# Kernel tuning notes

Hardware: AMD Instinct MI355X
Metric: run time of the kernel (lower is better)

The kernel has to match this reference:

```python
import jax, jax.numpy as jnp
import numpy as np

B, L, D, C = 8, 1024, 512, 4  # batch, maxlen, input_units(=output_unit), channel


def setup_inputs() -> dict:
    key = jax.random.key(0)
    ks = jax.random.split(key, 6)
    scale = 1.0 / np.sqrt(D)  # glorot-ish
    inputs = jax.random.normal(ks[0], (B, L, D), dtype=jnp.float32)
    pad_k = jnp.zeros((B, L, 1), dtype=jnp.float32)  # 0 = valid, -99999 = pad
    w_l = jax.random.normal(ks[1], (C, D, D), dtype=jnp.float32) * scale   # scalar_w per channel
    b_l = jnp.zeros((C,), dtype=jnp.float32)                                # scalar_b per channel
    w_v1 = jax.random.normal(ks[2], (C, D), dtype=jnp.float32) * scale     # vector_w1 [D,1] squeezed
    w_v2 = jax.random.normal(ks[3], (C, D, D), dtype=jnp.float32) * scale  # vector_w2
    b_v = jnp.zeros((C, D), dtype=jnp.float32)                              # vector_b [1,1,D] squeezed
    return {"inputs": inputs, "pad_k": pad_k, "w_l": w_l, "b_l": b_l,
            "w_v1": w_v1, "w_v2": w_v2, "b_v": b_v}


def reference(inputs, pad_k, w_l, b_l, w_v1, w_v2, b_v):
    # inputs: [B,L,D], pad_k: [B,L,1]. Dropout (mask_prob) is identity at inference.
    pad_k2 = (pad_k + 99999.0) / 99999.0              # [B,L,1], 1 at valid, 0 at pad
    pk = pad_k[:, None, :, 0]                          # [B,1,L]

    # --- scalar (pairwise bilinear) attention, all channels at once ---
    mat_l = jnp.einsum('bld,cde->bcle', inputs, w_l)   # [B,C,L,D]
    # M[b,c,i,j] = sum_d inputs[b,i,d] * mat_l[b,c,j,d] + b_l[c]
    M = jnp.einsum('bid,bcjd->bcij', inputs, mat_l) + b_l[None, :, None, None]
    A = jnp.tanh(M)                                    # [B,C,L,L]
    s = A.sum(axis=3)                                  # sum over j -> [B,C,L]
    a = jax.nn.softmax(pk + s, axis=-1)[..., None]     # softmax over L -> [B,C,L,1]

    # --- vector attention ---
    sb = jnp.tanh(jnp.einsum('bld,cde->bcle', inputs, w_v2) + b_v[None, :, None, :])  # [B,C,L,D]
    score_bar = jnp.einsum('bcld,cd->bcl', sb, w_v1) + pk                              # [B,C,L]
    a_bar = jax.nn.softmax(score_bar, axis=-1)                                         # [B,C,L]
    pooled = jnp.einsum('bcl,bld->bcd', a_bar, inputs)                                 # [B,C,D]

    # C_l = a_l * inputs + pooled(broadcast over L) * pad_k2
    C_l = a * inputs[:, None] + pooled[:, :, None, :] * pad_k2[:, None]                # [B,C,L,D]

    C_features = jnp.concatenate(
        [jnp.transpose(C_l, (0, 2, 3, 1)), inputs[..., None]], axis=-1)                # [B,L,D,C+1]
    return C_features, a, a_bar[..., None]
```

## Files before the change

### kernel.cpp

```cpp
#include <hip/hip_runtime.h>

#define BB 8
#define LL 1024
#define DD 512
#define CC 4

typedef unsigned short u16;
typedef unsigned int u32;
typedef __attribute__((ext_vector_type(8))) short bf16x8;
typedef __attribute__((ext_vector_type(4))) float f32x4;
typedef __attribute__((ext_vector_type(4))) unsigned short u16x4;
typedef __attribute__((ext_vector_type(4))) float float4v;

typedef __attribute__((address_space(1))) const u32 gu32;
typedef __attribute__((address_space(3))) u32 lu32;
typedef __attribute__((address_space(3))) u16 l16;

__device__ __forceinline__ void gload16(const void* g, void* l) {
  __builtin_amdgcn_global_load_lds((gu32*)g, (lu32*)l, 16, 0, 0);
}
__device__ __forceinline__ u32 lds_off(const u16* p) {
  return (u32)(uintptr_t)(l16*)p;
}

__device__ __forceinline__ u16 f2bf(float f) {
  unsigned u = __float_as_uint(f);
  u += 0x7FFF + ((u >> 16) & 1);
  return (u16)(u >> 16);
}
__device__ __forceinline__ float bf2f(u16 h) {
  return __uint_as_float(((unsigned)h) << 16);
}
__device__ __forceinline__ float fast_tanh(float x) {
  return 1.0f - 2.0f / (__expf(2.0f * x) + 1.0f);
}

__global__ __launch_bounds__(256) void k_split(const float4v* __restrict__ x,
                                               u16* __restrict__ hi, u16* __restrict__ lo) {
  int i = blockIdx.x * 256 + threadIdx.x;
  float4v v = x[i];
  u16x4 h, l;
#pragma unroll
  for (int k = 0; k < 4; ++k) {
    u16 hh = f2bf(v[k]);
    h[k] = hh;
    l[k] = f2bf(v[k] - bf2f(hh));
  }
  *(u16x4*)&hi[(size_t)i * 4] = h;
  *(u16x4*)&lo[(size_t)i * 4] = l;
}

__global__ __launch_bounds__(256) void k_tsplit(const float* __restrict__ w,
                                                u16* __restrict__ thi, u16* __restrict__ tlo) {
  __shared__ float t[32][33];
  int c = blockIdx.z;
  int tx = threadIdx.x;
  int ty = threadIdx.y;
  int e0 = blockIdx.x * 32, d0 = blockIdx.y * 32;
#pragma unroll
  for (int k = 0; k < 32; k += 8)
    t[ty + k][tx] = w[((size_t)c * DD + d0 + ty + k) * DD + e0 + tx];
  __syncthreads();
#pragma unroll
  for (int k = 0; k < 32; k += 8) {
    float v = t[tx][ty + k];
    size_t o = ((size_t)c * DD + e0 + ty + k) * DD + d0 + tx;
    u16 h = f2bf(v);
    thi[o] = h;
    if (tlo) tlo[o] = f2bf(v - bf2f(h));
  }
}

#define DSR(dst, addr, OFF) \
  asm volatile("ds_read_b128 %0, %1 offset:" #OFF : "=v"(dst) : "v"(addr))
#define LGKM(N) \
  do { __builtin_amdgcn_sched_barrier(0); \
       asm volatile("s_waitcnt lgkmcnt(" #N ")" ::: "memory"); \
       __builtin_amdgcn_sched_barrier(0); } while (0)

template<int NSEG, bool SPLIT>
__device__ __forceinline__ void gemm256(const u16* __restrict__ Ahi, const u16* __restrict__ Alo,
                                        const u16* __restrict__ Bhi, const u16* __restrict__ Blo,
                                        u16* lA, u16* lB, f32x4 (&acc)[8][4]) {
  const int tid = threadIdx.x;
  const int lane = tid & 63;
  const int wave = tid >> 6;
  const int wr = wave >> 2, wc = wave & 3;
  const int fr = lane & 15;
  const int fq = lane >> 4;
  const int xs = (tid & 7) ^ ((tid >> 3) & 7);
  const size_t soff = (size_t)(tid >> 3) * DD + (size_t)xs * 8;
  const int p0 = fq ^ (fr & 7);
  const int dk = ((p0 ^ 4) - p0) * 16;
  const u32 ra = lds_off(lA) + (u32)((wr * 128 + fr) * 128 + p0 * 16);
  const u32 rb = lds_off(lB) + (u32)((wc * 64 + fr) * 128 + p0 * 16);

  const int NT = NSEG * 8;

#define STAGE_TOP(T, beo) do {                                                \
    const int seg_ = SPLIT ? ((T) >> 3) : 0;                                  \
    const int kp_ = ((T) & 7) * 64;                                           \
    const u16* As_ = (SPLIT && seg_ == 1) ? Alo : Ahi;                        \
    const u16* Bs_ = (SPLIT && seg_ == 2) ? Blo : Bhi;                        \
    gload16(As_ + soff + kp_,                 lA + (beo) + tid * 8);          \
    gload16(Bs_ + soff + kp_,                 lB + (beo) + tid * 8);          \
    gload16(As_ + soff + (size_t)64 * DD + kp_, lA + (beo) + tid * 8 + 4096); \
    gload16(Bs_ + soff + (size_t)64 * DD + kp_, lB + (beo) + tid * 8 + 4096); \
  } while (0)

#define STAGE_MID(T, beo) do {                                                \
    const int seg_ = SPLIT ? ((T) >> 3) : 0;                                  \
    const int kp_ = ((T) & 7) * 64;                                           \
    const u16* As_ = (SPLIT && seg_ == 1) ? Alo : Ahi;                        \
    const u16* Bs_ = (SPLIT && seg_ == 2) ? Blo : Bhi;                        \
    gload16(As_ + soff + (size_t)128 * DD + kp_, lA + (beo) + tid * 8 + 8192);  \
    gload16(Bs_ + soff + (size_t)128 * DD + kp_, lB + (beo) + tid * 8 + 8192);  \
    gload16(As_ + soff + (size_t)192 * DD + kp_, lA + (beo) + tid * 8 + 12288); \
    gload16(Bs_ + soff + (size_t)192 * DD + kp_, lB + (beo) + tid * 8 + 12288); \
  } while (0)

#define MFMA2(m0, m1) do {                                                    \
    _Pragma("unroll")                                                         \
    for (int ni = 0; ni < 4; ++ni)                                            \
      acc[m0][ni] = __builtin_amdgcn_mfma_f32_16x16x32_bf16(                  \
          af[m0], bv[ni], acc[m0][ni], 0, 0, 0);                              \
    _Pragma("unroll")                                                         \
    for (int ni = 0; ni < 4; ++ni)                                            \
      acc[m1][ni] = __builtin_amdgcn_mfma_f32_16x16x32_bf16(                  \
          af[m1], bv[ni], acc[m1][ni], 0, 0, 0);                              \
  } while (0)

#define HALF(aA_, aB_) do {                                                   \
    bf16x8 af[8], bv[4];                                                      \
    DSR(bv[0], aB_, 0);    DSR(bv[1], aB_, 2048);                             \
    DSR(bv[2], aB_, 4096); DSR(bv[3], aB_, 6144);                             \
    DSR(af[0], aA_, 0);    DSR(af[1], aA_, 2048);                             \
    DSR(af[2], aA_, 4096); DSR(af[3], aA_, 6144);                             \
    LGKM(2);                                                                  \
    MFMA2(0, 1);                                                              \
    DSR(af[4], aA_, 8192); DSR(af[5], aA_, 10240);                            \
    LGKM(2);                                                                  \
    MFMA2(2, 3);                                                              \
    DSR(af[6], aA_, 12288); DSR(af[7], aA_, 14336);                           \
    LGKM(2);                                                                  \
    MFMA2(4, 5);                                                              \
    LGKM(0);                                                                  \
    MFMA2(6, 7);                                                              \
  } while (0)

#define HALF_MID(aA_, aB_, T, beo) do {                                       \
    bf16x8 af[8], bv[4];                                                      \
    DSR(bv[0], aB_, 0);    DSR(bv[1], aB_, 2048);                             \
    DSR(bv[2], aB_, 4096); DSR(bv[3], aB_, 6144);                             \
    DSR(af[0], aA_, 0);    DSR(af[1], aA_, 2048);                             \
    DSR(af[2], aA_, 4096); DSR(af[3], aA_, 6144);                             \
    LGKM(2);                                                                  \
    MFMA2(0, 1);                                                              \
    DSR(af[4], aA_, 8192); DSR(af[5], aA_, 10240);                            \
    LGKM(2);                                                                  \
    MFMA2(2, 3);                                                              \
    STAGE_MID(T, beo);                                                        \
    DSR(af[6], aA_, 12288); DSR(af[7], aA_, 14336);                           \
    LGKM(2);                                                                  \
    MFMA2(4, 5);                                                              \
    LGKM(0);                                                                  \
    MFMA2(6, 7);                                                              \
  } while (0)

  STAGE_TOP(0, 0);
  STAGE_MID(0, 0);
  int beN = 16384;
  u32 bo = 0;
#pragma unroll 1
  for (int t = 0; t < NT - 1; ++t) {
    __builtin_amdgcn_sched_barrier(0);
    asm volatile("s_waitcnt vmcnt(0)" ::: "memory");
    __builtin_amdgcn_sched_barrier(0);
    __builtin_amdgcn_s_barrier();
    __builtin_amdgcn_sched_barrier(0);
    STAGE_TOP(t + 1, beN);
    {
      u32 aA0 = ra + bo, aB0 = rb + bo;
      __builtin_amdgcn_s_setprio(1);
      HALF_MID(aA0, aB0, t + 1, beN);
      u32 aA1 = aA0 + dk, aB1 = aB0 + dk;
      HALF(aA1, aB1);
      __builtin_amdgcn_s_setprio(0);
    }
    beN ^= 16384;
    bo ^= 32768u;
  }
  __builtin_amdgcn_sched_barrier(0);
  asm volatile("s_waitcnt vmcnt(0)" ::: "memory");
  __builtin_amdgcn_sched_barrier(0);
  __builtin_amdgcn_s_barrier();
  __builtin_amdgcn_sched_barrier(0);
  {
    u32 aA0 = ra + bo, aB0 = rb + bo;
    __builtin_amdgcn_s_setprio(1);
    HALF(aA0, aB0);
    u32 aA1 = aA0 + dk, aB1 = aB0 + dk;
    HALF(aA1, aB1);
    __builtin_amdgcn_s_setprio(0);
  }
#undef STAGE_TOP
#undef STAGE_MID
#undef HALF
#undef HALF_MID
#undef MFMA2
}

__global__ __launch_bounds__(512, 2) void k_matl(const u16* __restrict__ Xhi, const u16* __restrict__ Xlo,
                                                 const u16* __restrict__ Whi, const u16* __restrict__ Wlo,
                                                 u16* __restrict__ mhi, u16* __restrict__ mlo) {
  __shared__ u16 lA[2 * 256 * 64];
  __shared__ u16 lB[2 * 256 * 64];
  int lin = blockIdx.x;
  int virt = (lin & 7) * 32 + (lin >> 3);
  int bc = virt >> 3, rem = virt & 7;
  int tm = rem >> 1, tn = rem & 1;
  int b = bc >> 2, c = bc & 3;
  const u16* Ahi = Xhi + (size_t)b * LL * DD + (size_t)tm * 256 * DD;
  const u16* Alo = Xlo + (size_t)b * LL * DD + (size_t)tm * 256 * DD;
  const u16* Bhi = Whi + (size_t)c * DD * DD + (size_t)tn * 256 * DD;
  const u16* Blo = Wlo + (size_t)c * DD * DD + (size_t)tn * 256 * DD;
  f32x4 acc[8][4];
#pragma unroll
  for (int mi = 0; mi < 8; ++mi)
#pragma unroll
    for (int ni = 0; ni < 4; ++ni) acc[mi][ni] = (f32x4){0.f, 0.f, 0.f, 0.f};
  gemm256<3, true>(Ahi, Alo, Bhi, Blo, lA, lB, acc);

  int lane = threadIdx.x & 63, wave = threadIdx.x >> 6;
  int wr = wave >> 2, wc = wave & 3;
  int rgrp = (lane >> 4) * 4, cidx = lane & 15;
#pragma unroll
  for (int mi = 0; mi < 8; ++mi)
#pragma unroll
    for (int ni = 0; ni < 4; ++ni) {
      int row = tm * 256 + wr * 128 + mi * 16 + rgrp;
      int col = tn * 256 + wc * 64 + ni * 16 + cidx;
#pragma unroll
      for (int j = 0; j < 4; ++j) {
        float v = acc[mi][ni][j];
        size_t o = ((size_t)bc * LL + row + j) * DD + col;
        u16 h = f2bf(v);
        mhi[o] = h;
        mlo[o] = f2bf(v - bf2f(h));
      }
    }
}

__global__ __launch_bounds__(512, 2) void k_s(const u16* __restrict__ Xhi, const u16* __restrict__ Xlo,
                                              const u16* __restrict__ mhi, const u16* __restrict__ mlo,
                                              const float* __restrict__ b_l, float* __restrict__ s_part) {
  __shared__ u16 lA[2 * 256 * 64];
  __shared__ u16 lB[2 * 256 * 64];
  int lin = blockIdx.x;
  int virt = (lin & 7) * 64 + (lin >> 3);
  int bc = virt >> 4, rem = virt & 15;
  int tm = rem >> 2, tn = rem & 3;
  int b = bc >> 2, c = bc & 3;
  const u16* Ahi = Xhi + (size_t)b * LL * DD + (size_t)tm * 256 * DD;
  const u16* Alo = Xlo + (size_t)b * LL * DD + (size_t)tm * 256 * DD;
  const u16* Bhi = mhi + (size_t)bc * LL * DD + (size_t)tn * 256 * DD;
  const u16* Blo = mlo + (size_t)bc * LL * DD + (size_t)tn * 256 * DD;
  f32x4 acc[8][4];
#pragma unroll
  for (int mi = 0; mi < 8; ++mi)
#pragma unroll
    for (int ni = 0; ni < 4; ++ni) acc[mi][ni] = (f32x4){0.f, 0.f, 0.f, 0.f};
  gemm256<3, true>(Ahi, Alo, Bhi, Blo, lA, lB, acc);

  int lane = threadIdx.x & 63, wave = threadIdx.x >> 6;
  int wr = wave >> 2, wc = wave & 3;
  float bl = b_l[c];
  float part[8][4];
#pragma unroll
  for (int mi = 0; mi < 8; ++mi)
#pragma unroll
    for (int j = 0; j < 4; ++j) part[mi][j] = 0.f;
#pragma unroll
  for (int mi = 0; mi < 8; ++mi)
#pragma unroll
    for (int ni = 0; ni < 4; ++ni)
#pragma unroll
      for (int j = 0; j < 4; ++j) part[mi][j] += fast_tanh(acc[mi][ni][j] + bl);
#pragma unroll
  for (int mi = 0; mi < 8; ++mi)
#pragma unroll
    for (int j = 0; j < 4; ++j) {
      float v = part[mi][j];
      v += __shfl_xor(v, 1, 64);
      v += __shfl_xor(v, 2, 64);
      v += __shfl_xor(v, 4, 64);
      v += __shfl_xor(v, 8, 64);
      part[mi][j] = v;
    }
  if ((lane & 15) == 0) {
    int slot = bc * 16 + tn * 4 + wc;
    int rg = (lane >> 4) * 4;
#pragma unroll
    for (int mi = 0; mi < 8; ++mi)
#pragma unroll
      for (int j = 0; j < 4; ++j) {
        int row = tm * 256 + wr * 128 + mi * 16 + rg + j;
        s_part[(size_t)slot * LL + row] = part[mi][j];
      }
  }
}

__global__ __launch_bounds__(512, 2) void k_sbar(const u16* __restrict__ Xhi, const u16* __restrict__ Wv2T,
                                                 const float* __restrict__ b_v, const float* __restrict__ w_v1,
                                                 float* __restrict__ sc_part) {
  __shared__ u16 lA[2 * 256 * 64];
  __shared__ u16 lB[2 * 256 * 64];
  int lin = blockIdx.x;
  int virt = (lin & 7) * 32 + (lin >> 3);
  int bc = virt >> 3, rem = virt & 7;
  int tm = rem >> 1, tn = rem & 1;
  int b = bc >> 2, c = bc & 3;
  const u16* Ahi = Xhi + (size_t)b * LL * DD + (size_t)tm * 256 * DD;
  const u16* Bhi = Wv2T + (size_t)c * DD * DD + (size_t)tn * 256 * DD;
  f32x4 acc[8][4];
#pragma unroll
  for (int mi = 0; mi < 8; ++mi)
#pragma unroll
    for (int ni = 0; ni < 4; ++ni) acc[mi][ni] = (f32x4){0.f, 0.f, 0.f, 0.f};
  gemm256<1, false>(Ahi, nullptr, Bhi, nullptr, lA, lB, acc);

  int lane = threadIdx.x & 63, wave = threadIdx.x >> 6;
  int wr = wave >> 2, wc = wave & 3;
  int cidx = lane & 15;
  float wv[4], bvv[4];
#pragma unroll
  for (int ni = 0; ni < 4; ++ni) {
    int col = tn * 256 + wc * 64 + ni * 16 + cidx;
    wv[ni] = w_v1[c * DD + col];
    bvv[ni] = b_v[c * DD + col];
  }
  float part[8][4];
#pragma unroll
  for (int mi = 0; mi < 8; ++mi)
#pragma unroll
    for (int j = 0; j < 4; ++j) part[mi][j] = 0.f;
#pragma unroll
  for (int mi = 0; mi < 8; ++mi)
#pragma unroll
    for (int ni = 0; ni < 4; ++ni)
#pragma unroll
      for (int j = 0; j < 4; ++j) part[mi][j] += fast_tanh(acc[mi][ni][j] + bvv[ni]) * wv[ni];
#pragma unroll
  for (int mi = 0; mi < 8; ++mi)
#pragma unroll
    for (int j = 0; j < 4; ++j) {
      float v = part[mi][j];
      v += __shfl_xor(v, 1, 64);
      v += __shfl_xor(v, 2, 64);
      v += __shfl_xor(v, 4, 64);
      v += __shfl_xor(v, 8, 64);
      part[mi][j] = v;
    }
  if ((lane & 15) == 0) {
    int slot = bc * 8 + tn * 4 + wc;
    int rg = (lane >> 4) * 4;
#pragma unroll
    for (int mi = 0; mi < 8; ++mi)
#pragma unroll
      for (int j = 0; j < 4; ++j) {
        int row = tm * 256 + wr * 128 + mi * 16 + rg + j;
        sc_part[(size_t)slot * LL + row] = part[mi][j];
      }
  }
}

__device__ __forceinline__ float blk_max(float v, float* red, int tid) {
#pragma unroll
  for (int m = 32; m >= 1; m >>= 1) v = fmaxf(v, __shfl_xor(v, m, 64));
  if ((tid & 63) == 0) red[tid >> 6] = v;
  __syncthreads();
  float r = red[0];
#pragma unroll
  for (int k = 1; k < 16; ++k) r = fmaxf(r, red[k]);
  __syncthreads();
  return r;
}
__device__ __forceinline__ float blk_sum(float v, float* red, int tid) {
#pragma unroll
  for (int m = 32; m >= 1; m >>= 1) v += __shfl_xor(v, m, 64);
  if ((tid & 63) == 0) red[tid >> 6] = v;
  __syncthreads();
  float r = red[0];
#pragma unroll
  for (int k = 1; k < 16; ++k) r += red[k];
  __syncthreads();
  return r;
}

__global__ __launch_bounds__(1024) void k_softmax(const float* __restrict__ s_part,
                                                  const float* __restrict__ sc_part,
                                                  const float* __restrict__ pad_k,
                                                  float* __restrict__ a_out,
                                                  float* __restrict__ abar_out) {
  __shared__ float red[16];
  int bc = blockIdx.x, b = bc >> 2;
  int i = threadIdx.x;
  float pk = pad_k[b * LL + i];

  float s = pk;
#pragma unroll
  for (int p = 0; p < 16; ++p) s += s_part[(size_t)(bc * 16 + p) * LL + i];
  float mx = blk_max(s, red, i);
  float e = expf(s - mx);
  float sum = blk_sum(e, red, i);
  a_out[bc * LL + i] = e / sum;

  float sb = pk;
#pragma unroll
  for (int p = 0; p < 8; ++p) sb += sc_part[(size_t)(bc * 8 + p) * LL + i];
  float mx2 = blk_max(sb, red, i);
  float e2 = expf(sb - mx2);
  float sum2 = blk_sum(e2, red, i);
  abar_out[bc * LL + i] = e2 / sum2;
}

__global__ __launch_bounds__(256) void k_pool2(const float* __restrict__ abar,
                                               const float* __restrict__ X,
                                               float* __restrict__ ppool) {
  __shared__ float w[4][32];
  int blk = blockIdx.x;
  int b = blk >> 5, ch = blk & 31;
  int t = threadIdx.x;
  if (t < 128)
    w[t >> 5][t & 31] = abar[(size_t)(b * 4 + (t >> 5)) * LL + ch * 32 + (t & 31)];
  __syncthreads();
  const float* xb = X + (size_t)b * LL * DD + (size_t)ch * 32 * DD;
  float a0[4] = {0.f, 0.f, 0.f, 0.f}, a1[4] = {0.f, 0.f, 0.f, 0.f};
  for (int j = 0; j < 32; ++j) {
    float x0 = xb[(size_t)j * DD + t];
    float x1 = xb[(size_t)j * DD + t + 256];
#pragma unroll
    for (int c = 0; c < 4; ++c) {
      float wv = w[c][j];
      a0[c] += wv * x0;
      a1[c] += wv * x1;
    }
  }
  size_t base = (size_t)blk * 4 * DD;
#pragma unroll
  for (int c = 0; c < 4; ++c) {
    ppool[base + c * DD + t] = a0[c];
    ppool[base + c * DD + t + 256] = a1[c];
  }
}

__global__ __launch_bounds__(512) void k_poolred(const float* __restrict__ ppool,
                                                 float* __restrict__ pooled) {
  int bc = blockIdx.x, b = bc >> 2, c = bc & 3;
  int d = threadIdx.x;
  float s = 0.f;
#pragma unroll 4
  for (int ch = 0; ch < 32; ++ch)
    s += ppool[((size_t)(b * 32 + ch) * 4 + c) * DD + d];
  pooled[bc * DD + d] = s;
}

__global__ __launch_bounds__(256) void k_assemble(const float* __restrict__ X,
                                                  const float* __restrict__ pad_k,
                                                  const float* __restrict__ a,
                                                  const float* __restrict__ pooled,
                                                  float* __restrict__ out) {
  __shared__ float buf[1280];
  int t = threadIdx.x;
  size_t idx = (size_t)blockIdx.x * 256 + t;
  int d = (int)(idx & (DD - 1));
  int bl = (int)(idx >> 9);
  int b = bl >> 10;
  int l = bl & (LL - 1);
  float x = X[idx];
  float pk2 = (pad_k[bl] + 99999.0f) * (1.0f / 99999.0f);
#pragma unroll
  for (int c = 0; c < 4; ++c) {
    float av = a[(size_t)(b * 4 + c) * LL + l];
    float pv = pooled[(size_t)(b * 4 + c) * DD + d];
    buf[t * 5 + c] = av * x + pv * pk2;
  }
  buf[t * 5 + 4] = x;
  __syncthreads();
  size_t base = (size_t)blockIdx.x * 1280;
#pragma unroll
  for (int k = 0; k < 5; ++k) out[base + k * 256 + t] = buf[k * 256 + t];
}

extern "C" void kernel_launch(void* const* d_in, const int* in_sizes, int n_in,
                              void* d_out, int out_size, void* d_ws, size_t ws_size,
                              hipStream_t stream) {
  (void)in_sizes; (void)n_in; (void)out_size;
  const float* X     = (const float*)d_in[0];
  const float* pad_k = (const float*)d_in[1];
  const float* w_l   = (const float*)d_in[2];
  const float* b_l   = (const float*)d_in[3];
  const float* w_v1  = (const float*)d_in[4];
  const float* w_v2  = (const float*)d_in[5];
  const float* b_v   = (const float*)d_in[6];
  float* out = (float*)d_out;

  char* wsp = (char*)d_ws;
  const size_t NEED = 28377088;
  bool small_ws = ws_size < NEED;
  u16* Xhi = (u16*)wsp;
  u16* Xlo = small_ws ? (u16*)((char*)d_out + 67108864)
                      : (u16*)(wsp + 8388608);
  size_t off = small_ws ? 8388608 : 16777216;
  u16* WlThi = (u16*)(wsp + off);  off += 2097152;
  u16* WlTlo = (u16*)(wsp + off);  off += 2097152;
  u16* Wv2T  = (u16*)(wsp + off);  off += 2097152;
  float* s_part  = (float*)(wsp + off); off += 2097152;
  float* sc_part = (float*)(wsp + off); off += 1048576;
  float* pooled  = (float*)(wsp + off); off += 65536;
  float* ppool   = (float*)(wsp + off); off += 2097152;

  u16* mhi = (u16*)d_out;
  u16* mlo = (u16*)d_out + 16777216;

  float* a_out    = out + 20971520;
  float* abar_out = out + 21004288;

  k_split<<<4096, 256, 0, stream>>>((const float4v*)X, Xhi, Xlo);
  k_tsplit<<<dim3(16, 16, 4), dim3(32, 8), 0, stream>>>(w_l, WlThi, WlTlo);
  k_tsplit<<<dim3(16, 16, 4), dim3(32, 8), 0, stream>>>(w_v2, Wv2T, nullptr);

  k_matl<<<256, 512, 0, stream>>>(Xhi, Xlo, WlThi, WlTlo, mhi, mlo);
  k_s<<<512, 512, 0, stream>>>(Xhi, Xlo, mhi, mlo, b_l, s_part);
  k_sbar<<<256, 512, 0, stream>>>(Xhi, Wv2T, b_v, w_v1, sc_part);

  k_softmax<<<32, 1024, 0, stream>>>(s_part, sc_part, pad_k, a_out, abar_out);
  k_pool2<<<256, 256, 0, stream>>>(abar_out, X, ppool);
  k_poolred<<<32, 512, 0, stream>>>(ppool, pooled);
  k_assemble<<<16384, 256, 0, stream>>>(X, pad_k, a_out, pooled, out);
}
```

Before: 214.2 us.

## Fuse hi/lo split-bf16 segments into one K loop with 32-wide tiles

```diff
diff --git a/kernel.cpp b/kernel.cpp
--- a/kernel.cpp
+++ b/kernel.cpp
@@ -78,143 +78,136 @@
        asm volatile("s_waitcnt lgkmcnt(" #N ")" ::: "memory"); \
        __builtin_amdgcn_sched_barrier(0); } while (0)
 
-template<int NSEG, bool SPLIT>
-__device__ __forceinline__ void gemm256(const u16* __restrict__ Ahi, const u16* __restrict__ Alo,
-                                        const u16* __restrict__ Bhi, const u16* __restrict__ Blo,
-                                        u16* lA, u16* lB, f32x4 (&acc)[8][4]) {
+template<bool SPLIT>
+__device__ __forceinline__ void gemm256f(const u16* __restrict__ Ahi, const u16* __restrict__ Alo,
+                                         const u16* __restrict__ Bhi, const u16* __restrict__ Blo,
+                                         u16* lA, u16* lB, f32x4 (&acc)[8][4]) {
   const int tid = threadIdx.x;
   const int lane = tid & 63;
   const int wave = tid >> 6;
   const int wr = wave >> 2, wc = wave & 3;
   const int fr = lane & 15;
   const int fq = lane >> 4;
-  const int xs = (tid & 7) ^ ((tid >> 3) & 7);
-  const size_t soff = (size_t)(tid >> 3) * DD + (size_t)xs * 8;
-  const int p0 = fq ^ (fr & 7);
-  const int dk = ((p0 ^ 4) - p0) * 16;
-  const u32 ra = lds_off(lA) + (u32)((wr * 128 + fr) * 128 + p0 * 16);
-  const u32 rb = lds_off(lB) + (u32)((wc * 64 + fr) * 128 + p0 * 16);
-
-  const int NT = NSEG * 8;
-
-#define STAGE_TOP(T, beo) do {                                                \
-    const int seg_ = SPLIT ? ((T) >> 3) : 0;                                  \
-    const int kp_ = ((T) & 7) * 64;                                           \
-    const u16* As_ = (SPLIT && seg_ == 1) ? Alo : Ahi;                        \
-    const u16* Bs_ = (SPLIT && seg_ == 2) ? Blo : Bhi;                        \
-    gload16(As_ + soff + kp_,                 lA + (beo) + tid * 8);          \
-    gload16(Bs_ + soff + kp_,                 lB + (beo) + tid * 8);          \
-    gload16(As_ + soff + (size_t)64 * DD + kp_, lA + (beo) + tid * 8 + 4096); \
-    gload16(Bs_ + soff + (size_t)64 * DD + kp_, lB + (beo) + tid * 8 + 4096); \
+  const int srow = tid >> 2;
+  const int xs = (tid & 3) ^ ((srow >> 1) & 3);
+  const size_t soff = (size_t)srow * DD + (size_t)xs * 8;
+  const int sidx = fq ^ ((fr >> 1) & 3);
+  const u32 ra = lds_off(lA) + (u32)((wr * 128 + fr) * 64 + sidx * 16);
+  const u32 rb = lds_off(lB) + (u32)((wc * 64 + fr) * 64 + sidx * 16);
+  const u32 BUFB = SPLIT ? 32768u : 16384u;
+
+#define STG_HI(T, beo) do {                                                   \
+    const int kp_ = (T) * 32;                                                 \
+    gload16(Ahi + soff + kp_,                  lA + (beo) + tid * 8);         \
+    gload16(Ahi + soff + (size_t)128 * DD + kp_, lA + (beo) + tid * 8 + 4096);\
+    gload16(Bhi + soff + kp_,                  lB + (beo) + tid * 8);         \
+    gload16(Bhi + soff + (size_t)128 * DD + kp_, lB + (beo) + tid * 8 + 4096);\
   } while (0)
 
-#define STAGE_MID(T, beo) do {                                                \
-    const int seg_ = SPLIT ? ((T) >> 3) : 0;                                  \
-    const int kp_ = ((T) & 7) * 64;                                           \
-    const u16* As_ = (SPLIT && seg_ == 1) ? Alo : Ahi;                        \
-    const u16* Bs_ = (SPLIT && seg_ == 2) ? Blo : Bhi;                        \
-    gload16(As_ + soff + (size_t)128 * DD + kp_, lA + (beo) + tid * 8 + 8192);  \
-    gload16(Bs_ + soff + (size_t)128 * DD + kp_, lB + (beo) + tid * 8 + 8192);  \
-    gload16(As_ + soff + (size_t)192 * DD + kp_, lA + (beo) + tid * 8 + 12288); \
-    gload16(Bs_ + soff + (size_t)192 * DD + kp_, lB + (beo) + tid * 8 + 12288); \
+#define STG_LO(T, beo) do {                                                   \
+    const int kp_ = (T) * 32;                                                 \
+    gload16(Alo + soff + kp_,                  lA + (beo) + 8192 + tid * 8);  \
+    gload16(Alo + soff + (size_t)128 * DD + kp_, lA + (beo) + 8192 + tid * 8 + 4096);\
+    gload16(Blo + soff + kp_,                  lB + (beo) + 8192 + tid * 8);  \
+    gload16(Blo + soff + (size_t)128 * DD + kp_, lB + (beo) + 8192 + tid * 8 + 4096);\
   } while (0)
 
-#define MFMA2(m0, m1) do {                                                    \
+#define MFMAC(A0, A1, BV) do {                                                \
     _Pragma("unroll")                                                         \
     for (int ni = 0; ni < 4; ++ni)                                            \
-      acc[m0][ni] = __builtin_amdgcn_mfma_f32_16x16x32_bf16(                  \
-          af[m0], bv[ni], acc[m0][ni], 0, 0, 0);                              \
+      acc[A0][ni] = __builtin_amdgcn_mfma_f32_16x16x32_bf16(                  \
+          af[A0], BV[ni], acc[A0][ni], 0, 0, 0);                              \
     _Pragma("unroll")                                                         \
     for (int ni = 0; ni < 4; ++ni)                                            \
-      acc[m1][ni] = __builtin_amdgcn_mfma_f32_16x16x32_bf16(                  \
-          af[m1], bv[ni], acc[m1][ni], 0, 0, 0);                              \
+      acc[A1][ni] = __builtin_amdgcn_mfma_f32_16x16x32_bf16(                  \
+          af[A1], BV[ni], acc[A1][ni], 0, 0, 0);                              \
   } while (0)
-
-#define HALF(aA_, aB_) do {                                                   \
-    bf16x8 af[8], bv[4];                                                      \
-    DSR(bv[0], aB_, 0);    DSR(bv[1], aB_, 2048);                             \
-    DSR(bv[2], aB_, 4096); DSR(bv[3], aB_, 6144);                             \
-    DSR(af[0], aA_, 0);    DSR(af[1], aA_, 2048);                             \
-    DSR(af[2], aA_, 4096); DSR(af[3], aA_, 6144);                             \
+#define MFMAL(i0, i1, AL, BV) do {                                            \
+    _Pragma("unroll")                                                         \
+    for (int ni = 0; ni < 4; ++ni)                                            \
+      acc[i0][ni] = __builtin_amdgcn_mfma_f32_16x16x32_bf16(                  \
+          AL[0], BV[ni], acc[i0][ni], 0, 0, 0);                               \
+    _Pragma("unroll")                                                         \
+    for (int ni = 0; ni < 4; ++ni)                                            \
+      acc[i1][ni] = __builtin_amdgcn_mfma_f32_16x16x32_bf16(                  \
+          AL[1], BV[ni], acc[i1][ni], 0, 0, 0);                               \
+  } while (0)
+
+#define COMP(bo_, MIDSTAGE, tn, beN_) do {                                    \
+    u32 aH_ = ra + (bo_), bH_ = rb + (bo_);                                   \
+    bf16x8 af[8], bh[4];                                                      \
+    DSR(bh[0], bH_, 0);    DSR(bh[1], bH_, 1024);                             \
+    DSR(bh[2], bH_, 2048); DSR(bh[3], bH_, 3072);                             \
+    DSR(af[0], aH_, 0);    DSR(af[1], aH_, 1024);                             \
+    DSR(af[2], aH_, 2048); DSR(af[3], aH_, 3072);                             \
     LGKM(2);                                                                  \
-    MFMA2(0, 1);                                                              \
-    DSR(af[4], aA_, 8192); DSR(af[5], aA_, 10240);                            \
+    __builtin_amdgcn_s_setprio(1);                                            \
+    MFMAC(0, 1, bh);                                                          \
+    DSR(af[4], aH_, 4096); DSR(af[5], aH_, 5120);                             \
     LGKM(2);                                                                  \
-    MFMA2(2, 3);                                                              \
-    DSR(af[6], aA_, 12288); DSR(af[7], aA_, 14336);                           \
+    MFMAC(2, 3, bh);                                                          \
+    if (MIDSTAGE) { STG_LO(tn, beN_); }                                       \
+    DSR(af[6], aH_, 6144); DSR(af[7], aH_, 7168);                             \
     LGKM(2);                                                                  \
-    MFMA2(4, 5);                                                              \
+    MFMAC(4, 5, bh);                                                          \
     LGKM(0);                                                                  \
-    MFMA2(6, 7);                                                              \
+    MFMAC(6, 7, bh);                                                          \
+    if (SPLIT) {                                                              \
+                                                \
+      bf16x8 bl[4];                                                           \
+      DSR(bl[0], bH_, 16384); DSR(bl[1], bH_, 17408);                         \
+      DSR(bl[2], bH_, 18432); DSR(bl[3], bH_, 19456);                         \
+      LGKM(0);                                                                \
+      MFMAC(0, 1, bl); MFMAC(2, 3, bl);                                       \
+      bf16x8 al0[2], al1[2], al2[2], al3[2];                                  \
+      DSR(al0[0], aH_, 16384); DSR(al0[1], aH_, 17408);                       \
+      DSR(al1[0], aH_, 18432); DSR(al1[1], aH_, 19456);                       \
+      MFMAC(4, 5, bl); MFMAC(6, 7, bl);                                       \
+                                                \
+      DSR(al2[0], aH_, 20480); DSR(al2[1], aH_, 21504);                       \
+      DSR(al3[0], aH_, 22528); DSR(al3[1], aH_, 23552);                       \
+      LGKM(4);                                                                \
+      MFMAL(0, 1, al0, bh); MFMAL(2, 3, al1, bh);                             \
+      LGKM(0);                                                                \
+      MFMAL(4, 5, al2, bh); MFMAL(6, 7, al3, bh);                             \
+    }                                                                         \
+    __builtin_amdgcn_s_setprio(0);                                            \
   } while (0)
 
-#define HALF_MID(aA_, aB_, T, beo) do {                                       \
-    bf16x8 af[8], bv[4];                                                      \
-    DSR(bv[0], aB_, 0);    DSR(bv[1], aB_, 2048);                             \
-    DSR(bv[2], aB_, 4096); DSR(bv[3], aB_, 6144);                             \
-    DSR(af[0], aA_, 0);    DSR(af[1], aA_, 2048);                             \
-    DSR(af[2], aA_, 4096); DSR(af[3], aA_, 6144);                             \
-    LGKM(2);                                                                  \
-    MFMA2(0, 1);                                                              \
-    DSR(af[4], aA_, 8192); DSR(af[5], aA_, 10240);                            \
-    LGKM(2);                                                                  \
-    MFMA2(2, 3);                                                              \
-    STAGE_MID(T, beo);                                                        \
-    DSR(af[6], aA_, 12288); DSR(af[7], aA_, 14336);                           \
-    LGKM(2);                                                                  \
-    MFMA2(4, 5);                                                              \
-    LGKM(0);                                                                  \
-    MFMA2(6, 7);                                                              \
-  } while (0)
-
-  STAGE_TOP(0, 0);
-  STAGE_MID(0, 0);
-  int beN = 16384;
+  STG_HI(0, 0);
+  if (SPLIT) STG_LO(0, 0);
+  u32 beN = SPLIT ? 16384u : 8192u;
   u32 bo = 0;
 #pragma unroll 1
-  for (int t = 0; t < NT - 1; ++t) {
+  for (int t = 0; t < 15; ++t) {
     __builtin_amdgcn_sched_barrier(0);
     asm volatile("s_waitcnt vmcnt(0)" ::: "memory");
     __builtin_amdgcn_sched_barrier(0);
     __builtin_amdgcn_s_barrier();
     __builtin_amdgcn_sched_barrier(0);
-    STAGE_TOP(t + 1, beN);
-    {
-      u32 aA0 = ra + bo, aB0 = rb + bo;
-      __builtin_amdgcn_s_setprio(1);
-      HALF_MID(aA0, aB0, t + 1, beN);
-      u32 aA1 = aA0 + dk, aB1 = aB0 + dk;
-      HALF(aA1, aB1);
-      __builtin_amdgcn_s_setprio(0);
-    }
-    beN ^= 16384;
-    bo ^= 32768u;
+    STG_HI(t + 1, beN);
+    COMP(bo, SPLIT ? 1 : 0, t + 1, beN);
+    beN ^= (SPLIT ? 16384u : 8192u);
+    bo ^= BUFB;
   }
   __builtin_amdgcn_sched_barrier(0);
   asm volatile("s_waitcnt vmcnt(0)" ::: "memory");
   __builtin_amdgcn_sched_barrier(0);
   __builtin_amdgcn_s_barrier();
   __builtin_amdgcn_sched_barrier(0);
-  {
-    u32 aA0 = ra + bo, aB0 = rb + bo;
-    __builtin_amdgcn_s_setprio(1);
-    HALF(aA0, aB0);
-    u32 aA1 = aA0 + dk, aB1 = aB0 + dk;
-    HALF(aA1, aB1);
-    __builtin_amdgcn_s_setprio(0);
-  }
-#undef STAGE_TOP
-#undef STAGE_MID
-#undef HALF
-#undef HALF_MID
-#undef MFMA2
+  COMP(bo, 0, 0, 0u);
+#undef STG_HI
+#undef STG_LO
+#undef COMP
+#undef MFMAC
+#undef MFMAL
 }
 
 __global__ __launch_bounds__(512, 2) void k_matl(const u16* __restrict__ Xhi, const u16* __restrict__ Xlo,
                                                  const u16* __restrict__ Whi, const u16* __restrict__ Wlo,
                                                  u16* __restrict__ mhi, u16* __restrict__ mlo) {
-  __shared__ u16 lA[2 * 256 * 64];
-  __shared__ u16 lB[2 * 256 * 64];
+  __shared__ u16 lA[2 * 2 * 256 * 32];
+  __shared__ u16 lB[2 * 2 * 256 * 32];
   int lin = blockIdx.x;
   int virt = (lin & 7) * 32 + (lin >> 3);
   int bc = virt >> 3, rem = virt & 7;
@@ -229,7 +222,7 @@
   for (int mi = 0; mi < 8; ++mi)
 #pragma unroll
     for (int ni = 0; ni < 4; ++ni) acc[mi][ni] = (f32x4){0.f, 0.f, 0.f, 0.f};
-  gemm256<3, true>(Ahi, Alo, Bhi, Blo, lA, lB, acc);
+  gemm256f<true>(Ahi, Alo, Bhi, Blo, lA, lB, acc);
 
   int lane = threadIdx.x & 63, wave = threadIdx.x >> 6;
   int wr = wave >> 2, wc = wave & 3;
@@ -254,8 +247,8 @@
 __global__ __launch_bounds__(512, 2) void k_s(const u16* __restrict__ Xhi, const u16* __restrict__ Xlo,
                                               const u16* __restrict__ mhi, const u16* __restrict__ mlo,
                                               const float* __restrict__ b_l, float* __restrict__ s_part) {
-  __shared__ u16 lA[2 * 256 * 64];
-  __shared__ u16 lB[2 * 256 * 64];
+  __shared__ u16 lA[2 * 2 * 256 * 32];
+  __shared__ u16 lB[2 * 2 * 256 * 32];
   int lin = blockIdx.x;
   int virt = (lin & 7) * 64 + (lin >> 3);
   int bc = virt >> 4, rem = virt & 15;
@@ -270,7 +263,7 @@
   for (int mi = 0; mi < 8; ++mi)
 #pragma unroll
     for (int ni = 0; ni < 4; ++ni) acc[mi][ni] = (f32x4){0.f, 0.f, 0.f, 0.f};
-  gemm256<3, true>(Ahi, Alo, Bhi, Blo, lA, lB, acc);
+  gemm256f<true>(Ahi, Alo, Bhi, Blo, lA, lB, acc);
 
   int lane = threadIdx.x & 63, wave = threadIdx.x >> 6;
   int wr = wave >> 2, wc = wave & 3;
@@ -313,8 +306,8 @@
 __global__ __launch_bounds__(512, 2) void k_sbar(const u16* __restrict__ Xhi, const u16* __restrict__ Wv2T,
                                                  const float* __restrict__ b_v, const float* __restrict__ w_v1,
                                                  float* __restrict__ sc_part) {
-  __shared__ u16 lA[2 * 256 * 64];
-  __shared__ u16 lB[2 * 256 * 64];
+  __shared__ u16 lA[2 * 256 * 32];
+  __shared__ u16 lB[2 * 256 * 32];
   int lin = blockIdx.x;
   int virt = (lin & 7) * 32 + (lin >> 3);
   int bc = virt >> 3, rem = virt & 7;
@@ -327,7 +320,7 @@
   for (int mi = 0; mi < 8; ++mi)
 #pragma unroll
     for (int ni = 0; ni < 4; ++ni) acc[mi][ni] = (f32x4){0.f, 0.f, 0.f, 0.f};
-  gemm256<1, false>(Ahi, nullptr, Bhi, nullptr, lA, lB, acc);
+  gemm256f<false>(Ahi, nullptr, Bhi, nullptr, lA, lB, acc);
 
   int lane = threadIdx.x & 63, wave = threadIdx.x >> 6;
   int wr = wave >> 2, wc = wave & 3;
```

Result: faster. 208.9 us (-2.5%).
